# Kernel tuning notes

Hardware: AMD Instinct MI355X
Metric: run time of the kernel (lower is better)

The kernel has to match this reference:

```python
import jax, jax.numpy as jnp
import numpy as np

D_MODEL = 2048
N_HEADS = 32
N_KV = 8
HEAD_DIM = D_MODEL // N_HEADS  # 64
MAX_POS = 4096
THETA = 10000.0


def setup_inputs() -> dict:
    key = jax.random.key(0)
    ks = jax.random.split(key, 6)
    b, s = 2, 2048
    hidden_states = jax.random.normal(ks[0], (b, s, D_MODEL), dtype=jnp.float32)
    attention_mask = jnp.ones((b, s), dtype=jnp.int32)
    position_ids = jnp.broadcast_to(jnp.arange(s, dtype=jnp.int32)[None, :], (b, s))
    sc = 0.02 / np.sqrt(D_MODEL)
    Wq = jax.random.normal(ks[1], (D_MODEL, N_HEADS * HEAD_DIM), dtype=jnp.float32) * sc
    Wk = jax.random.normal(ks[2], (D_MODEL, N_KV * HEAD_DIM), dtype=jnp.float32) * sc
    Wv = jax.random.normal(ks[3], (D_MODEL, N_KV * HEAD_DIM), dtype=jnp.float32) * sc
    Wo = jax.random.normal(ks[4], (D_MODEL, D_MODEL), dtype=jnp.float32) * sc
    return {"hidden_states": hidden_states, "attention_mask": attention_mask,
            "position_ids": position_ids, "Wq": Wq, "Wk": Wk, "Wv": Wv, "Wo": Wo}


def _rope(x, position_ids):
    # x: (b, s, h, d); rotate interleaved pairs (even, odd) as complex mult
    d = x.shape[-1]
    inv_freq = 1.0 / (THETA ** (jnp.arange(0, d, 2, dtype=jnp.float32) / d))  # (d/2,)
    angles = jnp.arange(MAX_POS, dtype=jnp.float32)[:, None] * inv_freq[None, :]  # (max_pos, d/2)
    cos = jnp.cos(angles)[position_ids][:, :, None, :]  # (b, s, 1, d/2)
    sin = jnp.sin(angles)[position_ids][:, :, None, :]
    xf = x.astype(jnp.float32).reshape(*x.shape[:-1], d // 2, 2)
    x0, x1 = xf[..., 0], xf[..., 1]
    o0 = x0 * cos - x1 * sin
    o1 = x0 * sin + x1 * cos
    return jnp.stack([o0, o1], axis=-1).reshape(x.shape).astype(x.dtype)


def reference(hidden_states, attention_mask, position_ids, Wq, Wk, Wv, Wo):
    b, s, _ = hidden_states.shape
    g = N_HEADS // N_KV
    xq = (hidden_states @ Wq).reshape(b, s, N_HEADS, HEAD_DIM)
    xk = (hidden_states @ Wk).reshape(b, s, N_KV, HEAD_DIM)
    xv = (hidden_states @ Wv).reshape(b, s, N_KV, HEAD_DIM)
    # GQA repeat: hkv -> (hkv g), matching einops.repeat ordering
    xk = jnp.repeat(xk, g, axis=2)  # (b, s, H, d)
    xv = jnp.repeat(xv, g, axis=2)
    xq = _rope(xq, position_ids)
    xk = _rope(xk, position_ids)
    scale = 1.0 / np.sqrt(HEAD_DIM)
    scores = jnp.einsum('bqhd,bkhd->bhqk', xq, xk) * scale  # (b, H, q, k)
    causal = jnp.tril(jnp.ones((s, s), dtype=bool))[None, None]  # (1,1,q,k)
    keep = causal & (attention_mask > 0)[:, None, None, :]
    neg = jnp.finfo(scores.dtype).min
    scores = jnp.where(keep, scores, neg)
    probs = jax.nn.softmax(scores, axis=-1)
    attn = jnp.einsum('bhqk,bkhd->bqhd', probs, xv).reshape(b, s, N_HEADS * HEAD_DIM)
    return attn @ Wo
```

## Files before the change

### kernel.cpp

```cpp
#include <hip/hip_runtime.h>
#include <math.h>

typedef unsigned short u16;
typedef __attribute__((ext_vector_type(8))) short short8;
typedef __attribute__((ext_vector_type(4))) float f32x4;
struct __align__(8) u16x4s { u16 x, y, z, w; };

__device__ __forceinline__ u16 f2bf(float f) {
  union { float f; unsigned u; } v; v.f = f;
  unsigned r = v.u + 0x7fffu + ((v.u >> 16) & 1u);
  return (u16)(r >> 16);
}

__device__ __forceinline__ void load_lds16(const u16* g, u16* l) {
  __builtin_amdgcn_global_load_lds((const __attribute__((address_space(1))) unsigned*)g,
                                   (__attribute__((address_space(3))) unsigned*)l, 16, 0, 0);
}

__global__ void prep_kernel(const int* __restrict__ amask,
                            float* __restrict__ rope_tab,
                            float* __restrict__ bias) {
  int idx = blockIdx.x * 256 + threadIdx.x;
  int pos = idx >> 5, i = idx & 31;
  float invf = (float)pow(10000.0, -(double)i / 32.0);
  float ang = (float)pos * invf;
  rope_tab[idx * 2]     = cosf(ang);
  rope_tab[idx * 2 + 1] = sinf(ang);
  if (idx < 4096) bias[idx] = (amask[idx] > 0) ? 0.f : -1e30f;
}

__global__ void convx_kernel(const float* __restrict__ X, u16* __restrict__ Xb) {
  int i = (blockIdx.x * 256 + threadIdx.x) * 4;
  float4 v = *(const float4*)&X[i];
  u16x4s o; o.x = f2bf(v.x); o.y = f2bf(v.y); o.z = f2bf(v.z); o.w = f2bf(v.w);
  *(u16x4s*)&Xb[i] = o;
}

__global__ void trans_kernel(const float* __restrict__ Wq, const float* __restrict__ Wk,
                             const float* __restrict__ Wv, const float* __restrict__ Wo,
                             u16* __restrict__ Wqt, u16* __restrict__ Wkt,
                             u16* __restrict__ Wvt, u16* __restrict__ Wot) {
  int t = blockIdx.x;
  const float* src; u16* dst; int N;
  if (t < 4096)       { src = Wq; dst = Wqt; N = 2048; }
  else if (t < 5120)  { src = Wk; dst = Wkt; N = 512;  t -= 4096; }
  else if (t < 6144)  { src = Wv; dst = Wvt; N = 512;  t -= 5120; }
  else                { src = Wo; dst = Wot; N = 2048; t -= 6144; }
  int ntn = N >> 5;
  int kt = t / ntn, nt = t - kt * ntn;
  __shared__ float tile[32][33];
  int tx = threadIdx.x & 31, ty = threadIdx.x >> 5;
#pragma unroll
  for (int r = 0; r < 32; r += 8)
    tile[ty + r][tx] = src[(size_t)(kt * 32 + ty + r) * N + nt * 32 + tx];
  __syncthreads();
#pragma unroll
  for (int r = 0; r < 32; r += 8)
    dst[(size_t)(nt * 32 + ty + r) * 2048 + kt * 32 + tx] = f2bf(tile[tx][ty + r]);
}

template<int EPI>
__global__ __launch_bounds__(256, 2) void gemm_kernel(
    const u16* __restrict__ A, const u16* __restrict__ B,
    u16* __restrict__ Qo, u16* __restrict__ Ko, u16* __restrict__ Vo,
    float* __restrict__ outf, int M, int N, int K,
    const float2* __restrict__ rope_tab, const int* __restrict__ pos_ids) {
  __shared__ __align__(16) u16 Ash[128 * 32];
  __shared__ __align__(16) u16 Bsh[128 * 32];
  const int tid = threadIdx.x;
  const int wave = tid >> 6, lane = tid & 63;
  const int c = lane & 15, g = lane >> 4;
  const int bm = blockIdx.y, bn = blockIdx.x;
  const int wm = (wave >> 1) * 64, wn = (wave & 1) * 64;

  f32x4 zf = {0.f, 0.f, 0.f, 0.f};
  f32x4 acc[4][4];
#pragma unroll
  for (int i = 0; i < 4; ++i)
#pragma unroll
    for (int j = 0; j < 4; ++j) acc[i][j] = zf;

  const int srow = wave * 32 + (lane >> 2);
  const int skoff = (lane & 3) * 8;
  const u16* Ag = A + (size_t)(bm * 128 + srow) * K + skoff;
  const u16* Bg = B + (size_t)(bn * 128 + srow) * K + skoff;
  const size_t rstep = (size_t)16 * K;
  u16* AsA0 = &Ash[(wave * 32) * 32];
  u16* AsA1 = &Ash[(wave * 32 + 16) * 32];
  u16* BsB0 = &Bsh[(wave * 32) * 32];
  u16* BsB1 = &Bsh[(wave * 32 + 16) * 32];

  for (int kk = 0; kk < K; kk += 32) {
    load_lds16(Ag + kk, AsA0);
    load_lds16(Ag + kk + rstep, AsA1);
    load_lds16(Bg + kk, BsB0);
    load_lds16(Bg + kk + rstep, BsB1);
    __syncthreads();
    short8 af[4], bfv[4];
#pragma unroll
    for (int i = 0; i < 4; ++i) af[i]  = *(const short8*)&Ash[(wm + i * 16 + c) * 32 + g * 8];
#pragma unroll
    for (int i = 0; i < 4; ++i) bfv[i] = *(const short8*)&Bsh[(wn + i * 16 + c) * 32 + g * 8];
#pragma unroll
    for (int i = 0; i < 4; ++i)
#pragma unroll
      for (int j = 0; j < 4; ++j)
        acc[i][j] = __builtin_amdgcn_mfma_f32_16x16x32_bf16(af[i], bfv[j], acc[i][j], 0, 0, 0);
    __syncthreads();
  }

  const int row0 = bm * 128 + wm + g * 4;
  const int colbase = bn * 128 + wn;
  const int col0 = colbase + c;
  if (EPI == 0) {
    if (colbase < 2560) {
      const bool isQ = colbase < 2048;
#pragma unroll
      for (int i = 0; i < 4; ++i) {
#pragma unroll
        for (int r = 0; r < 4; ++r) {
          const int row = row0 + i * 16 + r;
          const int pos = pos_ids[row];
#pragma unroll
          for (int j = 0; j < 4; ++j) {
            const int col = col0 + j * 16;
            float v = acc[i][j][r];
            float p = __shfl_xor(v, 1, 64);
            const float2 cs = rope_tab[pos * 32 + ((col & 63) >> 1)];
            float o = v * cs.x + ((lane & 1) ? p : -p) * cs.y;
            if (isQ) Qo[(size_t)row * 2048 + col] = f2bf(o * 0.125f);
            else     Ko[(size_t)row * 512 + (col - 2048)] = f2bf(o);
          }
        }
      }
    } else {
#pragma unroll
      for (int i = 0; i < 4; ++i) {
        const int srowv = row0 + i * 16;
        const int b_ = srowv >> 11, s_ = srowv & 2047;
#pragma unroll
        for (int j = 0; j < 4; ++j) {
          const int colv = col0 + j * 16 - 2560;
          u16x4s pk;
          pk.x = f2bf(acc[i][j][0]); pk.y = f2bf(acc[i][j][1]);
          pk.z = f2bf(acc[i][j][2]); pk.w = f2bf(acc[i][j][3]);
          *(u16x4s*)&Vo[((size_t)(b_ * 512 + colv)) * 2048 + s_] = pk;
        }
      }
    }
  } else {
#pragma unroll
    for (int i = 0; i < 4; ++i)
#pragma unroll
      for (int r = 0; r < 4; ++r) {
        const int row = row0 + i * 16 + r;
#pragma unroll
        for (int j = 0; j < 4; ++j)
          outf[(size_t)row * N + col0 + j * 16] = acc[i][j][r];
      }
  }
}

__global__ __launch_bounds__(256, 2) void attn_kernel(
    const u16* __restrict__ Qb,
    const u16* __restrict__ Kb,
    const u16* __restrict__ Vt,
    const float* __restrict__ bias,
    u16* __restrict__ Ob) {
  __shared__ __align__(16) u16 Ksh[64 * 64];
  __shared__ __align__(16) u16 Vsh[64 * 64];
  __shared__ __align__(16) u16 Plds[4][2][16 * 72];
  const int tid = threadIdx.x, wave = tid >> 6, lane = tid & 63;
  const int c = lane & 15, g = lane >> 4;
  const int h = blockIdx.y, b = blockIdx.z;
  const int hkv = h >> 2;
  const u16* Kbase = Kb + (size_t)b * 2048 * 512 + hkv * 64;
  const u16* Vbase = Vt + (size_t)(b * 8 + hkv) * 64 * 2048;
  const float* biasb = bias + b * 2048;
  const int sr = lane >> 3, scn = lane & 7;
  u16* Pw[2] = { &Plds[wave][0][0], &Plds[wave][1][0] };
  const f32x4 zf = {0.f, 0.f, 0.f, 0.f};

  for (int pass = 0; pass < 2; ++pass) {
    const int qtile = pass ? 15 - blockIdx.x : blockIdx.x;
    const int q0w = qtile * 128 + wave * 32;
    short8 qf[2][2];
#pragma unroll
    for (int sub = 0; sub < 2; ++sub) {
      const u16* Qrow = Qb + ((size_t)(b * 2048 + q0w + sub * 16 + c)) * 2048 + h * 64;
      qf[sub][0] = *(const short8*)&Qrow[g * 8];
      qf[sub][1] = *(const short8*)&Qrow[32 + g * 8];
    }
    f32x4 oa[2][4];
#pragma unroll
    for (int sub = 0; sub < 2; ++sub)
#pragma unroll
      for (int nb = 0; nb < 4; ++nb) oa[sub][nb] = zf;
    float lsum[2] = {0.f, 0.f};

    const int ktiles = 2 * qtile + 2;
    for (int kt = 0; kt < ktiles; ++kt) {
      const int kb = kt * 64;
      __syncthreads();
#pragma unroll
      for (int i = 0; i < 2; ++i) {
        const int rloc = i * 32 + wave * 8 + sr;
        const int cg = scn ^ (rloc & 7);
        load_lds16(Kbase + (size_t)(kb + rloc) * 512 + cg * 8, &Ksh[(i * 32 + wave * 8) * 64]);
        load_lds16(Vbase + (size_t)rloc * 2048 + kb + cg * 8, &Vsh[(i * 32 + wave * 8) * 64]);
      }
      __syncthreads();
      short8 kf[4][2];
#pragma unroll
      for (int blk = 0; blk < 4; ++blk) {
        const int rr = blk * 16 + c, sw = rr & 7;
        kf[blk][0] = *(const short8*)&Ksh[rr * 64 + ((0 + g) ^ sw) * 8];
        kf[blk][1] = *(const short8*)&Ksh[rr * 64 + ((4 + g) ^ sw) * 8];
      }
      f32x4 sc[2][4];
#pragma unroll
      for (int sub = 0; sub < 2; ++sub)
#pragma unroll
        for (int blk = 0; blk < 4; ++blk) {
          sc[sub][blk] = __builtin_amdgcn_mfma_f32_16x16x32_bf16(kf[blk][0], qf[sub][0], zf, 0, 0, 0);
          sc[sub][blk] = __builtin_amdgcn_mfma_f32_16x16x32_bf16(kf[blk][1], qf[sub][1], sc[sub][blk], 0, 0, 0);
        }
#pragma unroll
      for (int sub = 0; sub < 2; ++sub) {
        const int q0s = q0w + sub * 16;
        const bool needmask = (kb + 63 > q0s);
#pragma unroll
        for (int blk = 0; blk < 4; ++blk) {
          const float4 bv = *(const float4*)&biasb[kb + blk * 16 + g * 4];
          const float bva[4] = {bv.x, bv.y, bv.z, bv.w};
          float p[4];
#pragma unroll
          for (int r = 0; r < 4; ++r) {
            float v = sc[sub][blk][r] + bva[r];
            if (needmask && (kb + blk * 16 + g * 4 + r > q0s + c)) v = -3.0e30f;
            p[r] = __expf(v);
            lsum[sub] += p[r];
          }
          u16x4s pk; pk.x = f2bf(p[0]); pk.y = f2bf(p[1]); pk.z = f2bf(p[2]); pk.w = f2bf(p[3]);
          *(u16x4s*)&Pw[sub][c * 72 + blk * 16 + g * 4] = pk;
        }
      }
      short8 vf[4][2];
#pragma unroll
      for (int nb = 0; nb < 4; ++nb) {
        const int rr = nb * 16 + c, sw = rr & 7;
        vf[nb][0] = *(const short8*)&Vsh[rr * 64 + ((0 + g) ^ sw) * 8];
        vf[nb][1] = *(const short8*)&Vsh[rr * 64 + ((4 + g) ^ sw) * 8];
      }
#pragma unroll
      for (int sub = 0; sub < 2; ++sub)
#pragma unroll
        for (int st = 0; st < 2; ++st) {
          const short8 pf = *(const short8*)&Pw[sub][c * 72 + st * 32 + g * 8];
#pragma unroll
          for (int nb = 0; nb < 4; ++nb)
            oa[sub][nb] = __builtin_amdgcn_mfma_f32_16x16x32_bf16(pf, vf[nb][st], oa[sub][nb], 0, 0, 0);
        }
    }
#pragma unroll
    for (int sub = 0; sub < 2; ++sub) {
      float l = lsum[sub];
      l += __shfl_xor(l, 16, 64);
      l += __shfl_xor(l, 32, 64);
      float lr[4];
#pragma unroll
      for (int r = 0; r < 4; ++r) lr[r] = __shfl(l, g * 4 + r, 64);
      u16* Orow = Ob + ((size_t)(b * 2048 + q0w + sub * 16 + g * 4)) * 2048 + h * 64 + c;
#pragma unroll
      for (int r = 0; r < 4; ++r) {
        const float inv = 1.f / lr[r];
#pragma unroll
        for (int nb = 0; nb < 4; ++nb)
          Orow[(size_t)r * 2048 + nb * 16] = f2bf(oa[sub][nb][r] * inv);
      }
    }
  }
}

extern "C" void kernel_launch(void* const* d_in, const int* in_sizes, int n_in,
                              void* d_out, int out_size, void* d_ws, size_t ws_size,
                              hipStream_t stream) {
  const float* X   = (const float*)d_in[0];
  const int* amask = (const int*)d_in[1];
  const int* pos   = (const int*)d_in[2];
  const float* Wq  = (const float*)d_in[3];
  const float* Wk  = (const float*)d_in[4];
  const float* Wv  = (const float*)d_in[5];
  const float* Wo  = (const float*)d_in[6];
  float* out = (float*)d_out;

  char* ws = (char*)d_ws;
  size_t off = 0;
  auto alloc = [&](size_t bytes) { char* p = ws + off; off += (bytes + 255) & ~(size_t)255; return p; };
  u16* Xb   = (u16*)alloc(4096ull * 2048 * 2);
  u16* Wcat = (u16*)alloc(3072ull * 2048 * 2);
  u16* Wot  = (u16*)alloc(2048ull * 2048 * 2);
  u16* Qb   = (u16*)alloc(4096ull * 2048 * 2);
  u16* Kb   = (u16*)alloc(4096ull * 512 * 2);
  u16* Vt   = (u16*)alloc(2ull * 512 * 2048 * 2);
  u16* Ob   = (u16*)alloc(4096ull * 2048 * 2);
  float* rope = (float*)alloc(4096ull * 32 * 2 * 4);
  float* bias = (float*)alloc(4096ull * 4);
  u16* Wqt = Wcat;
  u16* Wkt = Wcat + 2048ull * 2048;
  u16* Wvt = Wcat + 2560ull * 2048;

  prep_kernel<<<512, 256, 0, stream>>>(amask, rope, bias);
  convx_kernel<<<8192, 256, 0, stream>>>(X, Xb);
  trans_kernel<<<10240, 256, 0, stream>>>(Wq, Wk, Wv, Wo, Wqt, Wkt, Wvt, Wot);
  gemm_kernel<0><<<dim3(24, 32), 256, 0, stream>>>(Xb, Wcat, Qb, Kb, Vt, nullptr,
                                                   4096, 3072, 2048, (const float2*)rope, pos);
  attn_kernel<<<dim3(8, 32, 2), 256, 0, stream>>>(Qb, Kb, Vt, bias, Ob);
  gemm_kernel<1><<<dim3(16, 32), 256, 0, stream>>>(Ob, Wot, nullptr, nullptr, nullptr, out,
                                                   4096, 2048, 2048, (const float2*)rope, pos);
}
```

Before: 330.6 us.

## Double-buffer K/V tiles in attention and pack RoPE epilogue stores

The attention kernel now keeps two LDS buffers for K and V. It issues the async global-to-LDS loads for the next key tile before computing on the current one, which leaves one barrier per iteration instead of two and is meant to hide load latency. Separately, the QKV GEMM epilogue computes RoPE pairs on even lanes only and writes two bf16 values as one 32-bit store, halving rope-table loads and store instructions. The cost is double the K/V LDS footprint, which could lower occupancy. The overlap also depends on where the compiler places its vmcnt waits.

New measurement: 346.8 us. 1.05x slower.

```diff
diff --git a/kernel.cpp b/kernel.cpp
--- a/kernel.cpp
+++ b/kernel.cpp
@@ -115,6 +115,7 @@
   if (EPI == 0) {
     if (colbase < 2560) {
       const bool isQ = colbase < 2048;
+      const bool evenlane = !(lane & 1);
 #pragma unroll
       for (int i = 0; i < 4; ++i) {
 #pragma unroll
@@ -126,10 +127,15 @@
             const int col = col0 + j * 16;
             float v = acc[i][j][r];
             float p = __shfl_xor(v, 1, 64);
-            const float2 cs = rope_tab[pos * 32 + ((col & 63) >> 1)];
-            float o = v * cs.x + ((lane & 1) ? p : -p) * cs.y;
-            if (isQ) Qo[(size_t)row * 2048 + col] = f2bf(o * 0.125f);
-            else     Ko[(size_t)row * 512 + (col - 2048)] = f2bf(o);
+            if (evenlane) {
+              const float2 cs = rope_tab[pos * 32 + ((col & 63) >> 1)];
+              float o0 = v * cs.x - p * cs.y;
+              float o1 = v * cs.y + p * cs.x;
+              if (isQ) { o0 *= 0.125f; o1 *= 0.125f; }
+              const unsigned pk = (unsigned)f2bf(o0) | ((unsigned)f2bf(o1) << 16);
+              if (isQ) *(unsigned*)&Qo[(size_t)row * 2048 + col] = pk;
+              else     *(unsigned*)&Ko[(size_t)row * 512 + (col - 2048)] = pk;
+            }
           }
         }
       }
@@ -167,8 +173,8 @@
     const u16* __restrict__ Vt,
     const float* __restrict__ bias,
     u16* __restrict__ Ob) {
-  __shared__ __align__(16) u16 Ksh[64 * 64];
-  __shared__ __align__(16) u16 Vsh[64 * 64];
+  __shared__ __align__(16) u16 Ksh[2][64 * 64];
+  __shared__ __align__(16) u16 Vsh[2][64 * 64];
   __shared__ __align__(16) u16 Plds[4][2][16 * 72];
   const int tid = threadIdx.x, wave = tid >> 6, lane = tid & 63;
   const int c = lane & 15, g = lane >> 4;
@@ -199,23 +205,34 @@
     float lsum[2] = {0.f, 0.f};
 
     const int ktiles = 2 * qtile + 2;
+    __syncthreads();
+#pragma unroll
+    for (int i = 0; i < 2; ++i) {
+      const int rloc = i * 32 + wave * 8 + sr;
+      const int cg = scn ^ (rloc & 7);
+      load_lds16(Kbase + (size_t)rloc * 512 + cg * 8, &Ksh[0][(i * 32 + wave * 8) * 64]);
+      load_lds16(Vbase + (size_t)rloc * 2048 + cg * 8, &Vsh[0][(i * 32 + wave * 8) * 64]);
+    }
     for (int kt = 0; kt < ktiles; ++kt) {
       const int kb = kt * 64;
+      const int cur = kt & 1;
       __syncthreads();
-#pragma unroll
-      for (int i = 0; i < 2; ++i) {
-        const int rloc = i * 32 + wave * 8 + sr;
-        const int cg = scn ^ (rloc & 7);
-        load_lds16(Kbase + (size_t)(kb + rloc) * 512 + cg * 8, &Ksh[(i * 32 + wave * 8) * 64]);
-        load_lds16(Vbase + (size_t)rloc * 2048 + kb + cg * 8, &Vsh[(i * 32 + wave * 8) * 64]);
-      }
-      __syncthreads();
+      if (kt + 1 < ktiles) {
+        const int kbn = kb + 64;
+#pragma unroll
+        for (int i = 0; i < 2; ++i) {
+          const int rloc = i * 32 + wave * 8 + sr;
+          const int cg = scn ^ (rloc & 7);
+          load_lds16(Kbase + (size_t)(kbn + rloc) * 512 + cg * 8, &Ksh[cur ^ 1][(i * 32 + wave * 8) * 64]);
+          load_lds16(Vbase + (size_t)rloc * 2048 + kbn + cg * 8, &Vsh[cur ^ 1][(i * 32 + wave * 8) * 64]);
+        }
+      }
       short8 kf[4][2];
 #pragma unroll
       for (int blk = 0; blk < 4; ++blk) {
         const int rr = blk * 16 + c, sw = rr & 7;
-        kf[blk][0] = *(const short8*)&Ksh[rr * 64 + ((0 + g) ^ sw) * 8];
-        kf[blk][1] = *(const short8*)&Ksh[rr * 64 + ((4 + g) ^ sw) * 8];
+        kf[blk][0] = *(const short8*)&Ksh[cur][rr * 64 + ((0 + g) ^ sw) * 8];
+        kf[blk][1] = *(const short8*)&Ksh[cur][rr * 64 + ((4 + g) ^ sw) * 8];
       }
       f32x4 sc[2][4];
 #pragma unroll
@@ -249,8 +266,8 @@
 #pragma unroll
       for (int nb = 0; nb < 4; ++nb) {
         const int rr = nb * 16 + c, sw = rr & 7;
-        vf[nb][0] = *(const short8*)&Vsh[rr * 64 + ((0 + g) ^ sw) * 8];
-        vf[nb][1] = *(const short8*)&Vsh[rr * 64 + ((4 + g) ^ sw) * 8];
+        vf[nb][0] = *(const short8*)&Vsh[cur][rr * 64 + ((0 + g) ^ sw) * 8];
+        vf[nb][1] = *(const short8*)&Vsh[cur][rr * 64 + ((4 + g) ^ sw) * 8];
       }
 #pragma unroll
       for (int sub = 0; sub < 2; ++sub)
```
